# Optimization experiments

Hardware: AMD Instinct MI355X
Metric: run time of the kernel (lower is better)

Reference implementation:

```python
import jax, jax.numpy as jnp
import numpy as np

NUM_ITERATIONS = 3


def squash(t, axis=-1):
    # scale = |t|^2 / (1 + |t|^2); out = scale * t / |t|  (matches torch source exactly)
    norm = jnp.sum(t * t, axis=axis, keepdims=True)
    scale = norm / (1.0 + norm)
    return scale * t / jnp.sqrt(norm)


def setup_inputs() -> dict:
    key = jax.random.key(0)
    k_u, k_w = jax.random.split(key)
    B, K, R, M, P = 1024, 2, 2336, 4, 16
    u = jax.random.normal(k_u, (B, R, M), dtype=jnp.float32)
    W = jax.random.normal(k_w, (K, R, M, P), dtype=jnp.float32)
    return {"u": u, "W": W}


def reference(u, W):
    # u: [B, R, M]; W: [K, R, M, P]
    # torch: matmul(u[:,None,:,None,:], W) -> [B,K,R,1,P]; we drop the singleton dim.
    u_ji = jnp.einsum('brm,krmp->bkrp', u, W)  # [B, K, R, P]
    b = jnp.zeros_like(u_ji)
    v = None
    for i in range(NUM_ITERATIONS):
        c = jax.nn.softmax(b, axis=2)                      # softmax over routes
        v = squash(jnp.sum(c * u_ji, axis=2, keepdims=True))  # [B, K, 1, P]
        if i != NUM_ITERATIONS - 1:
            b = b + jnp.sum(u_ji * v, axis=-1, keepdims=True)  # agreement, broadcasts over P
    v = jnp.squeeze(v, axis=2)                 # [B, K, P]
    classes = jnp.sqrt(jnp.sum(v * v, axis=-1))  # [B, K]
    return classes
```

## Files before the change

### kernel.cpp

```cpp
#include <hip/hip_runtime.h>
#include <hip/hip_fp16.h>
#include <math.h>


#define THREADS 512
#define NWAVE 8
#define RR 2336
#define KK 2

#if __has_builtin(__builtin_amdgcn_fdot2)
typedef _Float16 h2v __attribute__((ext_vector_type(2)));
static __device__ __forceinline__ float dot2h(__half2 a, __half2 b, float c) {
    h2v av, bv;
    __builtin_memcpy(&av, &a, 4);
    __builtin_memcpy(&bv, &b, 4);
    return __builtin_amdgcn_fdot2(av, bv, c, false);
}
#else
static __device__ __forceinline__ float dot2h(__half2 a, __half2 b, float c) {
    float2 fa = __half22float2(a), fb = __half22float2(b);
    return fmaf(fa.x, fb.x, fmaf(fa.y, fb.y, c));
}
#endif

__global__ __launch_bounds__(256)
void w_repack_kernel(const float* __restrict__ W, __half2* __restrict__ Wt)
{
    const int n = KK * RR * 8;
    for (int j = blockIdx.x * 256 + threadIdx.x; j < n; j += gridDim.x * 256) {
        const int p2 = j & 7;
        const int rk = j >> 3;
        const float* wp = W + (size_t)rk * 64;
        const float x0 = wp[0*16 + 2*p2],     x1 = wp[1*16 + 2*p2];
        const float x2 = wp[2*16 + 2*p2],     x3 = wp[3*16 + 2*p2];
        const float y0 = wp[0*16 + 2*p2 + 1], y1 = wp[1*16 + 2*p2 + 1];
        const float y2 = wp[2*16 + 2*p2 + 1], y3 = wp[3*16 + 2*p2 + 1];
        __half2* o = Wt + (size_t)j * 4;
        o[0] = __floats2half2_rn(x0, x1);
        o[1] = __floats2half2_rn(x2, x3);
        o[2] = __floats2half2_rn(y0, y1);
        o[3] = __floats2half2_rn(y2, y3);
    }
}

#define STREAM_COMP(base, i, uu, wv)                                   \
    {                                                                  \
        const int r = (base) + (i) * 64 + rbase;                       \
        const __half2 u01 = __floats2half2_rn(uu.x, uu.y);             \
        const __half2 u23 = __floats2half2_rn(uu.z, uu.w);             \
        const __half2* hm = (const __half2*)&wv;                       \
        const float ax = dot2h(u01, hm[0], dot2h(u23, hm[1], 0.0f));   \
        const float ay = dot2h(u01, hm[2], dot2h(u23, hm[3], 0.0f));   \
        sA += ax; sB += ay;                                            \
        *(__half2*)(uji + r * 16 + p2 * 2) = __floats2half2_rn(ax, ay); \
    }

__global__ __launch_bounds__(THREADS, 2)
void caps_routing_kernel(const float* __restrict__ u,
                         const __half2* __restrict__ Wt,
                         float* __restrict__ out)
{
    __shared__ __half uji[RR * 16];
    __shared__ float  red[2][NWAVE][17];

    const int bi   = blockIdx.x;
    const int b    = bi >> 1;
    const int k    = bi & 1;
    const int tid  = threadIdx.x;
    const int lane = tid & 63;
    const int wave = tid >> 6;
    const int p2   = lane & 7;
    const int g    = lane >> 3;

    const float4* __restrict__ u4p = (const float4*)u;
    const float4* __restrict__ w4t = (const float4*)Wt + (size_t)k * RR * 8 + p2;

    float sA = 0.0f, sB = 0.0f;
    {
        const int rbase = wave * 8 + g;
        float4 uuA_n = u4p[b * RR + rbase];
        float4 wvA_n = w4t[(size_t)rbase * 8];
        float4 uuB_n = u4p[b * RR + 768 + rbase];
        float4 wvB_n = w4t[(size_t)(768 + rbase) * 8];
        float4 uuC_n = u4p[b * RR + 1536 + rbase];
        float4 wvC_n = w4t[(size_t)(1536 + rbase) * 8];
        #pragma unroll 3
        for (int i = 0; i < 12; ++i) {
            const float4 uuA = uuA_n, wvA = wvA_n;
            const float4 uuB = uuB_n, wvB = wvB_n;
            const float4 uuC = uuC_n, wvC = wvC_n;
            if (i + 1 < 12) {
                const int ra = (i + 1) * 64 + rbase;
                uuA_n = u4p[b * RR + ra];
                wvA_n = w4t[(size_t)ra * 8];
                const int rb = 768 + (i + 1) * 64 + rbase;
                uuB_n = u4p[b * RR + rb];
                wvB_n = w4t[(size_t)rb * 8];
                const int rc = 1536 + (i + 1) * 64 + rbase;
                uuC_n = u4p[b * RR + rc];
                wvC_n = w4t[(size_t)rc * 8];
            }
            STREAM_COMP(0,    i, uuA, wvA)
            STREAM_COMP(768,  i, uuB, wvB)
            STREAM_COMP(1536, i, uuC, wvC)
        }
        if (wave < 4) {
            const int r = 2304 + rbase;
            const float4 uu = u4p[b * RR + r];
            const float4 wv = w4t[(size_t)r * 8];
            const __half2 u01 = __floats2half2_rn(uu.x, uu.y);
            const __half2 u23 = __floats2half2_rn(uu.z, uu.w);
            const __half2* hm = (const __half2*)&wv;
            const float ax = dot2h(u01, hm[0], dot2h(u23, hm[1], 0.0f));
            const float ay = dot2h(u01, hm[2], dot2h(u23, hm[3], 0.0f));
            sA += ax; sB += ay;
            *(__half2*)(uji + r * 16 + p2 * 2) = __floats2half2_rn(ax, ay);
        }
    }
    sA += __shfl_xor(sA, 8);  sB += __shfl_xor(sB, 8);
    sA += __shfl_xor(sA, 16); sB += __shfl_xor(sB, 16);
    sA += __shfl_xor(sA, 32); sB += __shfl_xor(sB, 32);
    if (lane < 8) {
        red[0][wave][2 * p2]     = sA;
        red[0][wave][2 * p2 + 1] = sB;
    }
    __syncthreads();

    float vcum[8];

    {
        float col = 0.0f;
        if (lane < 16) {
            #pragma unroll
            for (int w = 0; w < NWAVE; ++w) col += red[0][w][lane];
        }
        float nr = col * col;
        nr += __shfl_xor(nr, 1);
        nr += __shfl_xor(nr, 2);
        nr += __shfl_xor(nr, 4);
        nr += __shfl_xor(nr, 8);
        const float inv  = 1.0f / (float)RR;
        const float norm = nr * inv * inv;
        const float f    = sqrtf(norm) / (1.0f + norm);
        const float vnew = col * inv * f;
        #pragma unroll
        for (int i = 0; i < 8; ++i) vcum[i] = __shfl(vnew, (lane & 1) * 8 + i);
    }

    #pragma unroll 1
    for (int it = 1; it < 3; ++it) {
        const int buf = it & 1;

        __half2 v2[4];
        #pragma unroll
        for (int i = 0; i < 4; ++i) v2[i] = __floats2half2_rn(vcum[2*i], vcum[2*i+1]);

        float4 raw[10];
        #pragma unroll
        for (int s = 0; s < 10; ++s) {
            int row = s * 256 + wave * 32 + (lane >> 1);
            row = (row < RR) ? row : (RR - 1);
            raw[s] = *(const float4*)((const char*)uji + row * 32 + (lane & 1) * 16);
        }

        float s8[8] = {0,0,0,0,0,0,0,0};
        float se = 0.0f;
        #pragma unroll
        for (int s = 0; s < 10; ++s) {
            const bool ok = (s * 256 + wave * 32 + (lane >> 1)) < RR;
            const __half2* hp = (const __half2*)&raw[s];
            float d = dot2h(hp[0], v2[0],
                      dot2h(hp[1], v2[1],
                      dot2h(hp[2], v2[2],
                      dot2h(hp[3], v2[3], 0.0f))));
            d += __shfl_xor(d, 1);
            float e = ok ? __expf(d) : 0.0f;
            se += e;
            #pragma unroll
            for (int q = 0; q < 4; ++q) {
                float2 f = __half22float2(hp[q]);
                s8[2*q]   = fmaf(f.x, e, s8[2*q]);
                s8[2*q+1] = fmaf(f.y, e, s8[2*q+1]);
            }
        }

        #pragma unroll
        for (int o = 2; o <= 32; o <<= 1) {
            se += __shfl_xor(se, o);
            #pragma unroll
            for (int i = 0; i < 8; ++i) s8[i] += __shfl_xor(s8[i], o);
        }
        if (lane < 2) {
            #pragma unroll
            for (int i = 0; i < 8; ++i) red[buf][wave][(lane & 1) * 8 + i] = s8[i];
            if (lane == 0) red[buf][wave][16] = se;
        }
        __syncthreads();

        {
            float col = 0.0f;
            if (lane < 17) {
                #pragma unroll
                for (int w = 0; w < NWAVE; ++w) col += red[buf][w][lane];
            }
            float nr = col * col;
            nr += __shfl_xor(nr, 1);
            nr += __shfl_xor(nr, 2);
            nr += __shfl_xor(nr, 4);
            nr += __shfl_xor(nr, 8);
            const float se_t = __shfl(col, 16);
            const float inv  = 1.0f / se_t;
            const float norm = nr * inv * inv;
            if (it == 1) {
                const float f    = sqrtf(norm) / (1.0f + norm);
                const float vnew = col * inv * f;
                #pragma unroll
                for (int i = 0; i < 8; ++i) vcum[i] += __shfl(vnew, (lane & 1) * 8 + i);
            } else if (wave == 0 && lane == 0) {
                out[b * KK + k] = norm / (1.0f + norm);
            }
        }
    }
}

extern "C" void kernel_launch(void* const* d_in, const int* in_sizes, int n_in,
                              void* d_out, int out_size, void* d_ws, size_t ws_size,
                              hipStream_t stream) {
    const float* u = (const float*)d_in[0];
    const float* W = (const float*)d_in[1];
    float* out = (float*)d_out;
    __half2* Wt = (__half2*)d_ws;

    w_repack_kernel<<<dim3(256), dim3(256), 0, stream>>>(W, Wt);
    caps_routing_kernel<<<dim3(2048), dim3(THREADS), 0, stream>>>(u, Wt, out);
}
```

Measured before the change: 127.6 us.

## Use DPP/swizzle/permlane reductions, hoist u_ji LDS loads, raise occupancy bound

Replaces the __shfl_xor butterfly reductions with DPP row operations, ds_swizzle and permlane32_swap, which should cut the LDS-routed shuffle cost. The u_ji rows are loaded from LDS into registers once and reused across both routing iterations, and the tail row is handled only by wave 0 with no clamp or mask. The routing vector is broadcast through a small shared array instead of per-lane shuffles, and launch bounds change from 2 to 4 blocks per CU. The main risks are extra register pressure from keeping raw[] live across iterations, which could cause spills under the tighter bound, and possible lane-pattern mistakes in the DPP controls.

```diff
diff --git a/kernel.cpp b/kernel.cpp
--- a/kernel.cpp
+++ b/kernel.cpp
@@ -21,6 +21,31 @@
     float2 fa = __half22float2(a), fb = __half22float2(b);
     return fmaf(fa.x, fb.x, fmaf(fa.y, fb.y, c));
 }
+#endif
+
+#define DPP_XOR1 0xB1
+#define DPP_XOR2 0x4E
+#define DPP_ROR4 0x124
+#define DPP_ROR8 0x128
+
+template <int CTRL>
+static __device__ __forceinline__ float dpp_addf(float x) {
+    const int y = __builtin_amdgcn_update_dpp(0, __float_as_int(x), CTRL, 0xf, 0xf, true);
+    return x + __int_as_float(y);
+}
+static __device__ __forceinline__ float swz16_addf(float x) {
+    const int y = __builtin_amdgcn_ds_swizzle(__float_as_int(x), 0x401f);
+    return x + __int_as_float(y);
+}
+#if __has_builtin(__builtin_amdgcn_permlane32_swap)
+static __device__ __forceinline__ float pl32_addf(float x) {
+    typedef unsigned uv2 __attribute__((ext_vector_type(2)));
+    const uv2 r = __builtin_amdgcn_permlane32_swap(__float_as_uint(x), __float_as_uint(x),
+                                                   false, false);
+    return __uint_as_float(r[0]) + __uint_as_float(r[1]);
+}
+#else
+static __device__ __forceinline__ float pl32_addf(float x) { return x + __shfl_xor(x, 32); }
 #endif
 
 __global__ __launch_bounds__(256)
@@ -55,13 +80,32 @@
         *(__half2*)(uji + r * 16 + p2 * 2) = __floats2half2_rn(ax, ay); \
     }
 
-__global__ __launch_bounds__(THREADS, 2)
+#define SWEEP_STEP(rw)                                                     \
+    {                                                                      \
+        const __half2* hp = (const __half2*)&(rw);                         \
+        float d = dot2h(hp[0], v2[0], dot2h(hp[1], v2[1],                  \
+                  dot2h(hp[2], v2[2], dot2h(hp[3], v2[3], 0.0f))));        \
+        d = dpp_addf<DPP_XOR1>(d);             \
+        const float e = __expf(d);           \
+        se += e;                                                           \
+        { const float2 f0 = __half22float2(hp[0]);                         \
+          s8[0] = fmaf(f0.x, e, s8[0]); s8[1] = fmaf(f0.y, e, s8[1]); }    \
+        { const float2 f1 = __half22float2(hp[1]);                         \
+          s8[2] = fmaf(f1.x, e, s8[2]); s8[3] = fmaf(f1.y, e, s8[3]); }    \
+        { const float2 f2 = __half22float2(hp[2]);                         \
+          s8[4] = fmaf(f2.x, e, s8[4]); s8[5] = fmaf(f2.y, e, s8[5]); }    \
+        { const float2 f3 = __half22float2(hp[3]);                         \
+          s8[6] = fmaf(f3.x, e, s8[6]); s8[7] = fmaf(f3.y, e, s8[7]); }    \
+    }
+
+__global__ __launch_bounds__(THREADS, 4)
 void caps_routing_kernel(const float* __restrict__ u,
                          const __half2* __restrict__ Wt,
                          float* __restrict__ out)
 {
-    __shared__ __half uji[RR * 16];
-    __shared__ float  red[2][NWAVE][17];
+    __shared__ __align__(16) __half uji[RR * 16];
+    __shared__ __align__(16) float  red[2][NWAVE][20];
+    __shared__ __align__(16) float  vrow[2][16];
 
     const int bi   = blockIdx.x;
     const int b    = bi >> 1;
@@ -117,34 +161,39 @@
             *(__half2*)(uji + r * 16 + p2 * 2) = __floats2half2_rn(ax, ay);
         }
     }
-    sA += __shfl_xor(sA, 8);  sB += __shfl_xor(sB, 8);
-    sA += __shfl_xor(sA, 16); sB += __shfl_xor(sB, 16);
-    sA += __shfl_xor(sA, 32); sB += __shfl_xor(sB, 32);
+    sA = dpp_addf<DPP_ROR8>(sA);  sB = dpp_addf<DPP_ROR8>(sB);
+    sA = swz16_addf(sA);          sB = swz16_addf(sB);
+    sA = pl32_addf(sA);           sB = pl32_addf(sB);
     if (lane < 8) {
         red[0][wave][2 * p2]     = sA;
         red[0][wave][2 * p2 + 1] = sB;
     }
     __syncthreads();
 
-    float vcum[8];
-
+    float vcum_s;
     {
         float col = 0.0f;
-        if (lane < 16) {
-            #pragma unroll
-            for (int w = 0; w < NWAVE; ++w) col += red[0][w][lane];
-        }
+        #pragma unroll
+        for (int w = 0; w < NWAVE; ++w) col += red[0][w][lane & 15];
         float nr = col * col;
-        nr += __shfl_xor(nr, 1);
-        nr += __shfl_xor(nr, 2);
-        nr += __shfl_xor(nr, 4);
-        nr += __shfl_xor(nr, 8);
+        nr = dpp_addf<DPP_XOR1>(nr);
+        nr = dpp_addf<DPP_XOR2>(nr);
+        nr = dpp_addf<DPP_ROR4>(nr);
+        nr = dpp_addf<DPP_ROR8>(nr);
         const float inv  = 1.0f / (float)RR;
         const float norm = nr * inv * inv;
         const float f    = sqrtf(norm) / (1.0f + norm);
-        const float vnew = col * inv * f;
-        #pragma unroll
-        for (int i = 0; i < 8; ++i) vcum[i] = __shfl(vnew, (lane & 1) * 8 + i);
+        vcum_s = col * inv * f;
+        if (lane < 16) vrow[0][lane] = vcum_s;
+    }
+
+    float4 raw[9], raw9;
+    {
+        const int rb = wave * 32 + (lane >> 1);
+        #pragma unroll
+        for (int s = 0; s < 9; ++s)
+            raw[s] = *(const float4*)((const char*)uji + (s * 256 + rb) * 32 + (lane & 1) * 16);
+        raw9 = *(const float4*)((const char*)uji + (2304 + (lane >> 1)) * 32 + (lane & 1) * 16);
     }
 
     #pragma unroll 1
@@ -152,70 +201,60 @@
         const int buf = it & 1;
 
         __half2 v2[4];
-        #pragma unroll
-        for (int i = 0; i < 4; ++i) v2[i] = __floats2half2_rn(vcum[2*i], vcum[2*i+1]);
-
-        float4 raw[10];
-        #pragma unroll
-        for (int s = 0; s < 10; ++s) {
-            int row = s * 256 + wave * 32 + (lane >> 1);
-            row = (row < RR) ? row : (RR - 1);
-            raw[s] = *(const float4*)((const char*)uji + row * 32 + (lane & 1) * 16);
-        }
-
-        float s8[8] = {0,0,0,0,0,0,0,0};
-        float se = 0.0f;
-        #pragma unroll
-        for (int s = 0; s < 10; ++s) {
-            const bool ok = (s * 256 + wave * 32 + (lane >> 1)) < RR;
-            const __half2* hp = (const __half2*)&raw[s];
-            float d = dot2h(hp[0], v2[0],
-                      dot2h(hp[1], v2[1],
-                      dot2h(hp[2], v2[2],
-                      dot2h(hp[3], v2[3], 0.0f))));
-            d += __shfl_xor(d, 1);
-            float e = ok ? __expf(d) : 0.0f;
-            se += e;
+        {
+            const float2* vp = (const float2*)vrow[buf ^ 1];
             #pragma unroll
             for (int q = 0; q < 4; ++q) {
-                float2 f = __half22float2(hp[q]);
-                s8[2*q]   = fmaf(f.x, e, s8[2*q]);
-                s8[2*q+1] = fmaf(f.y, e, s8[2*q+1]);
-            }
-        }
-
-        #pragma unroll
-        for (int o = 2; o <= 32; o <<= 1) {
-            se += __shfl_xor(se, o);
+                const float2 pv = vp[(lane & 1) * 4 + q];
+                v2[q] = __floats2half2_rn(pv.x, pv.y);
+            }
+        }
+
+        float s8[8] = {0, 0, 0, 0, 0, 0, 0, 0};
+        float se = 0.0f;
+        #pragma unroll
+        for (int s = 0; s < 9; ++s) SWEEP_STEP(raw[s])
+        if (wave == 0) SWEEP_STEP(raw9)
+
+        #pragma unroll
+        for (int i = 0; i < 8; ++i) {
+            s8[i] = dpp_addf<DPP_XOR2>(s8[i]);
+            s8[i] = dpp_addf<DPP_ROR4>(s8[i]);
+            s8[i] = dpp_addf<DPP_ROR8>(s8[i]);
+            s8[i] = swz16_addf(s8[i]);
+            s8[i] = pl32_addf(s8[i]);
+        }
+        se = dpp_addf<DPP_XOR2>(se);
+        se = dpp_addf<DPP_ROR4>(se);
+        se = dpp_addf<DPP_ROR8>(se);
+        se = swz16_addf(se);
+        se = pl32_addf(se);
+
+        if (lane < 2) {
+            *(float4*)&red[buf][wave][(lane & 1) * 8]     = make_float4(s8[0], s8[1], s8[2], s8[3]);
+            *(float4*)&red[buf][wave][(lane & 1) * 8 + 4] = make_float4(s8[4], s8[5], s8[6], s8[7]);
+            if (lane == 0) red[buf][wave][16] = se;
+        }
+        __syncthreads();
+
+        {
+            float col = 0.0f, set = 0.0f;
             #pragma unroll
-            for (int i = 0; i < 8; ++i) s8[i] += __shfl_xor(s8[i], o);
-        }
-        if (lane < 2) {
-            #pragma unroll
-            for (int i = 0; i < 8; ++i) red[buf][wave][(lane & 1) * 8 + i] = s8[i];
-            if (lane == 0) red[buf][wave][16] = se;
-        }
-        __syncthreads();
-
-        {
-            float col = 0.0f;
-            if (lane < 17) {
-                #pragma unroll
-                for (int w = 0; w < NWAVE; ++w) col += red[buf][w][lane];
+            for (int w = 0; w < NWAVE; ++w) {
+                col += red[buf][w][lane & 15];
+                set += red[buf][w][16];
             }
             float nr = col * col;
-            nr += __shfl_xor(nr, 1);
-            nr += __shfl_xor(nr, 2);
-            nr += __shfl_xor(nr, 4);
-            nr += __shfl_xor(nr, 8);
-            const float se_t = __shfl(col, 16);
-            const float inv  = 1.0f / se_t;
+            nr = dpp_addf<DPP_XOR1>(nr);
+            nr = dpp_addf<DPP_XOR2>(nr);
+            nr = dpp_addf<DPP_ROR4>(nr);
+            nr = dpp_addf<DPP_ROR8>(nr);
+            const float inv  = 1.0f / set;
             const float norm = nr * inv * inv;
             if (it == 1) {
-                const float f    = sqrtf(norm) / (1.0f + norm);
-                const float vnew = col * inv * f;
-                #pragma unroll
-                for (int i = 0; i < 8; ++i) vcum[i] += __shfl(vnew, (lane & 1) * 8 + i);
+                const float f = sqrtf(norm) / (1.0f + norm);
+                vcum_s += col * inv * f;
+                if (lane < 16) vrow[1][lane] = vcum_s;
             } else if (wave == 0 && lane == 0) {
                 out[b * KK + k] = norm / (1.0f + norm);
             }
```

New measurement: 143.9 us. +12.8%, slower.
